# Performance work log

Hardware: AMD Instinct MI355X
Metric: run time of the kernel (lower is better)

The kernel has to match this reference:

```python
import jax, jax.numpy as jnp
import numpy as np

N_NODES = 100000
N_EDGES = 1200000
C = 64            # hidden_channels == in_channels
HEADS = 4
HEAD_D = C // HEADS
EDGE_D = 16
N_LAYERS = 3
NUM_GRAPHS = 128


def setup_inputs() -> dict:
    key = jax.random.key(0)
    ks = jax.random.split(key, 24)
    x = jax.random.normal(ks[0], (N_NODES, C), dtype=jnp.float32)
    edge_index = jax.random.randint(ks[1], (2, N_EDGES), 0, N_NODES, dtype=jnp.int64)
    edge_attr = jax.random.normal(ks[2], (N_EDGES, EDGE_D), dtype=jnp.float32)
    batch = jnp.sort(jax.random.randint(ks[3], (N_NODES,), 0, NUM_GRAPHS, dtype=jnp.int64))
    s = 1.0 / np.sqrt(C)
    se = 1.0 / np.sqrt(EDGE_D)
    inp = {
        "x": x, "edge_index": edge_index, "edge_attr": edge_attr, "batch": batch,
        "Wq": jax.random.normal(ks[4], (N_LAYERS, C, C), jnp.float32) * s,
        "bq": jnp.zeros((N_LAYERS, C), jnp.float32),
        "Wk": jax.random.normal(ks[5], (N_LAYERS, C, C), jnp.float32) * s,
        "bk": jnp.zeros((N_LAYERS, C), jnp.float32),
        "Wv": jax.random.normal(ks[6], (N_LAYERS, C, C), jnp.float32) * s,
        "bv": jnp.zeros((N_LAYERS, C), jnp.float32),
        "We": jax.random.normal(ks[7], (N_LAYERS, EDGE_D, C), jnp.float32) * se,
        "be": jnp.zeros((N_LAYERS, C), jnp.float32),
        "Wskip": jax.random.normal(ks[8], (N_LAYERS, C, C), jnp.float32) * s,
        "bskip": jnp.zeros((N_LAYERS, C), jnp.float32),
        "lin1_w": jax.random.normal(ks[9], (C, C), jnp.float32) * s,
        "lin1_b": jnp.zeros((C,), jnp.float32),
        "lin2_w": jax.random.normal(ks[10], (C, 1), jnp.float32) * s,
        "lin2_b": jnp.zeros((1,), jnp.float32),
    }
    return inp


def _transformer_conv(x, src, dst, edge_attr, Wq, bq, Wk, bk, Wv, bv, We, be, Ws, bs):
    """PyG-style TransformerConv: edge-softmax attention with edge features."""
    n = x.shape[0]
    e = src.shape[0]
    q = (x @ Wq + bq)[dst].reshape(e, HEADS, HEAD_D)          # query at target i
    ea = (edge_attr @ We + be).reshape(e, HEADS, HEAD_D)      # shared edge proj
    k = (x @ Wk + bk)[src].reshape(e, HEADS, HEAD_D) + ea
    v = (x @ Wv + bv)[src].reshape(e, HEADS, HEAD_D) + ea
    logit = jnp.einsum('ehd,ehd->eh', q, k) / jnp.sqrt(jnp.float32(HEAD_D))  # [E,H]
    # numerically-stable softmax over edges sharing the same destination node
    m = jax.ops.segment_max(logit, dst, num_segments=n)       # [N,H]
    ex = jnp.exp(logit - m[dst])
    denom = jax.ops.segment_sum(ex, dst, num_segments=n)      # [N,H]
    alpha = ex / jnp.maximum(denom[dst], 1e-16)
    agg = jax.ops.segment_sum(alpha[:, :, None] * v, dst, num_segments=n)   # [N,H,D]
    return agg.reshape(n, HEADS * HEAD_D) + x @ Ws + bs       # root/skip weight


def reference(x, edge_index, edge_attr, batch, Wq, bq, Wk, bk, Wv, bv, We, be,
              Wskip, bskip, lin1_w, lin1_b, lin2_w, lin2_b):
    src, dst = edge_index[0], edge_index[1]
    h = x
    for l in range(N_LAYERS):
        h = _transformer_conv(h, src, dst, edge_attr,
                              Wq[l], bq[l], Wk[l], bk[l], Wv[l], bv[l],
                              We[l], be[l], Wskip[l], bskip[l])
        if l < N_LAYERS - 1:
            h = jax.nn.relu(h)
    # global mean pool over graphs
    sums = jax.ops.segment_sum(h, batch, num_segments=NUM_GRAPHS)            # [G,C]
    cnt = jax.ops.segment_sum(jnp.ones((h.shape[0], 1), h.dtype), batch,
                              num_segments=NUM_GRAPHS)
    pooled = sums / jnp.maximum(cnt, 1.0)
    out = jax.nn.relu(pooled @ lin1_w + lin1_b)
    return (out @ lin2_w + lin2_b).squeeze(-1)                               # [G]
```

## Files before the change

kernel.cpp:

```cpp
#include <hip/hip_runtime.h>
#include <hip/hip_bf16.h>

#define NODES_C 64
#define HEADS 4
#define HEAD_D 16

__global__ void count_k(const int* __restrict__ dst, int E, int* __restrict__ deg) {
    int e = blockIdx.x * blockDim.x + threadIdx.x;
    if (e < E) atomicAdd(&deg[dst[e]], 1);
}

__global__ __launch_bounds__(1024) void scan_chunk(const int* __restrict__ deg,
                                                   int* __restrict__ excl,
                                                   int* __restrict__ chunkSums, int N) {
    __shared__ int buf[1024];
    int i = blockIdx.x * 1024 + threadIdx.x;
    int v = (i < N) ? deg[i] : 0;
    buf[threadIdx.x] = v;
    __syncthreads();
    for (int off = 1; off < 1024; off <<= 1) {
        int t = (threadIdx.x >= off) ? buf[threadIdx.x - off] : 0;
        __syncthreads();
        buf[threadIdx.x] += t;
        __syncthreads();
    }
    if (i < N) excl[i] = buf[threadIdx.x] - v;
    if (threadIdx.x == 1023) chunkSums[blockIdx.x] = buf[1023];
}

__global__ __launch_bounds__(128) void scan_sums(int* __restrict__ chunkSums, int nChunks) {
    __shared__ int buf[128];
    int v = (threadIdx.x < nChunks) ? chunkSums[threadIdx.x] : 0;
    buf[threadIdx.x] = v;
    __syncthreads();
    for (int off = 1; off < 128; off <<= 1) {
        int t = (threadIdx.x >= off) ? buf[threadIdx.x - off] : 0;
        __syncthreads();
        buf[threadIdx.x] += t;
        __syncthreads();
    }
    if (threadIdx.x < nChunks) chunkSums[threadIdx.x] = buf[threadIdx.x] - v;
}

__global__ void scan_add(int* __restrict__ excl, const int* __restrict__ chunkSums,
                         int N, int E) {
    int i = blockIdx.x * blockDim.x + threadIdx.x;
    if (i < N) excl[i] += chunkSums[i >> 10];
    if (i == 0) excl[N] = E;
}

__global__ void fill_k(const int* __restrict__ dst, int E,
                       const int* __restrict__ row_start, int* __restrict__ cursor,
                       int* __restrict__ csr) {
    int e = blockIdx.x * blockDim.x + threadIdx.x;
    if (e < E) {
        int d = dst[e];
        int pos = atomicAdd(&cursor[d], 1);
        csr[row_start[d] + pos] = e;
    }
}

__global__ void gather_edges(const int* __restrict__ csr, const int* __restrict__ srcA,
                             const float4* __restrict__ ea4,
                             int* __restrict__ csr_src, float4* __restrict__ csr_ea,
                             int E) {
    int t = blockIdx.x * blockDim.x + threadIdx.x;
    int p = t >> 2, q = t & 3;
    if (p < E) {
        int e = csr[p];
        if (q == 0) csr_src[p] = srcA[e];
        csr_ea[(size_t)p * 4 + q] = ea4[(size_t)e * 4 + q];
    }
}

#define GB 16
__global__ __launch_bounds__(256) void gemm_qkvs(
    const float* __restrict__ Hin,
    const float* __restrict__ Wq, const float* __restrict__ bq,
    const float* __restrict__ Wk, const float* __restrict__ bk,
    const float* __restrict__ Wv, const float* __restrict__ bv,
    const float* __restrict__ Ws, const float* __restrict__ bs,
    float* __restrict__ Q, float* __restrict__ KV,
    float* __restrict__ Ssk, int N)
{
    int m = threadIdx.x >> 6;
    int c = threadIdx.x & 63;
    const float* W = (m == 0) ? Wq : (m == 1) ? Wk : (m == 2) ? Wv : Ws;
    const float* b = (m == 0) ? bq : (m == 1) ? bk : (m == 2) ? bv : bs;
    float* Out     = (m == 0) ? Q  : (m == 3) ? Ssk : KV;
    size_t rowStride = (m == 1 || m == 2) ? 128 : 64;
    int cOff = (m == 1) ? 2 * c : (m == 2) ? 2 * c + 1 : c;

    float wcol[64];
#pragma unroll
    for (int t = 0; t < 64; ++t) wcol[t] = W[t * 64 + c];
    float bias = b[c];

    __shared__ __align__(16) float hrow[GB][64];

    for (int base = blockIdx.x * GB; base < N; base += gridDim.x * GB) {
        int nn = min(GB, N - base);
        __syncthreads();
        for (int idx = threadIdx.x; idx < nn * 64; idx += 256)
            hrow[idx >> 6][idx & 63] = Hin[base * 64 + idx];
        __syncthreads();
        for (int r = 0; r < nn; ++r) {
            const float4* h4 = (const float4*)hrow[r];
            float acc = bias;
#pragma unroll
            for (int t4 = 0; t4 < 16; ++t4) {
                float4 hv = h4[t4];
                acc += hv.x * wcol[4 * t4 + 0];
                acc += hv.y * wcol[4 * t4 + 1];
                acc += hv.z * wcol[4 * t4 + 2];
                acc += hv.w * wcol[4 * t4 + 3];
            }
            Out[(size_t)(base + r) * rowStride + cOff] = acc;
        }
    }
}

__global__ __launch_bounds__(256) void attn_pre(
    const float* __restrict__ Q, const float2* __restrict__ KV,
    const float* __restrict__ Ssk,
    const int* __restrict__ row_start, const int* __restrict__ csr_src,
    const float* __restrict__ csr_ea,
    const float* __restrict__ We, const float* __restrict__ be,
    float* __restrict__ Hout, int N, int doRelu)
{
    __shared__ float weS[16 * 68];
    for (int idx = threadIdx.x; idx < 1024; idx += 256)
        weS[(idx >> 6) * 68 + (idx & 63)] = We[idx];
    __syncthreads();

    int lane = threadIdx.x & 63;
    int tl = lane & 15;
    int hb = lane & 48;
    float wcol[16];
#pragma unroll
    for (int t = 0; t < 16; ++t) wcol[t] = weS[t * 68 + lane];
    float beL = be[lane];

    int gwave  = (blockIdx.x * blockDim.x + threadIdx.x) >> 6;
    int nwaves = (gridDim.x * blockDim.x) >> 6;

    for (int i = gwave; i < N; i += nwaves) {
        float q = Q[(size_t)i * 64 + lane];

        const float4* qh4 = (const float4*)(Q + (size_t)i * 64 + hb);
        const float4* wr4 = (const float4*)(weS + tl * 68 + hb);
        float4 qa = qh4[0], qb4 = qh4[1], qc4 = qh4[2], qd = qh4[3];
        float4 wa = wr4[0], wb = wr4[1], wc4 = wr4[2], wd = wr4[3];
        float G = qa.x * wa.x + qa.y * wa.y + qa.z * wa.z + qa.w * wa.w
                + qb4.x * wb.x + qb4.y * wb.y + qb4.z * wb.z + qb4.w * wb.w
                + qc4.x * wc4.x + qc4.y * wc4.y + qc4.z * wc4.z + qc4.w * wc4.w
                + qd.x * wd.x + qd.y * wd.y + qd.z * wd.z + qd.w * wd.w;
        float rb = q * beL;
#pragma unroll
        for (int off = 8; off >= 1; off >>= 1) rb += __shfl_xor(rb, off, 16);
        float qbase = rb * 0.25f;

        int beg = row_start[i], end = row_start[i + 1];
        float m = -INFINITY, s = 0.f, acc = 0.f, z = 0.f;

        int p = beg;
        for (; p + 3 < end; p += 4) {
            int j0 = csr_src[p],     j1 = csr_src[p + 1];
            int j2 = csr_src[p + 2], j3 = csr_src[p + 3];
            float2 kv0 = KV[(size_t)j0 * 64 + lane];
            float2 kv1 = KV[(size_t)j1 * 64 + lane];
            float2 kv2 = KV[(size_t)j2 * 64 + lane];
            float2 kv3 = KV[(size_t)j3 * 64 + lane];
            float a0 = csr_ea[(size_t)p * 16 + tl];
            float a1 = csr_ea[(size_t)p * 16 + 16 + tl];
            float a2 = csr_ea[(size_t)p * 16 + 32 + tl];
            float a3 = csr_ea[(size_t)p * 16 + 48 + tl];

            float l0 = q * kv0.x + a0 * G;
            float l1 = q * kv1.x + a1 * G;
            float l2 = q * kv2.x + a2 * G;
            float l3 = q * kv3.x + a3 * G;
#pragma unroll
            for (int off = 8; off >= 1; off >>= 1) {
                l0 += __shfl_xor(l0, off, 16);
                l1 += __shfl_xor(l1, off, 16);
                l2 += __shfl_xor(l2, off, 16);
                l3 += __shfl_xor(l3, off, 16);
            }
            l0 = l0 * 0.25f + qbase;
            l1 = l1 * 0.25f + qbase;
            l2 = l2 * 0.25f + qbase;
            l3 = l3 * 0.25f + qbase;

            float nm = fmaxf(fmaxf(fmaxf(l0, l1), fmaxf(l2, l3)), m);
            float sc = __expf(m - nm);
            float w0 = __expf(l0 - nm), w1 = __expf(l1 - nm);
            float w2 = __expf(l2 - nm), w3 = __expf(l3 - nm);
            s   = s * sc + w0 + w1 + w2 + w3;
            acc = acc * sc + w0 * kv0.y + w1 * kv1.y + w2 * kv2.y + w3 * kv3.y;
            z   = z * sc + w0 * a0 + w1 * a1 + w2 * a2 + w3 * a3;
            m = nm;
        }
        for (; p < end; ++p) {
            int j = csr_src[p];
            float2 kv = KV[(size_t)j * 64 + lane];
            float a = csr_ea[(size_t)p * 16 + tl];
            float l = q * kv.x + a * G;
#pragma unroll
            for (int off = 8; off >= 1; off >>= 1) l += __shfl_xor(l, off, 16);
            l = l * 0.25f + qbase;
            float nm = fmaxf(m, l);
            float sc = __expf(m - nm);
            float w  = __expf(l - nm);
            s   = s * sc + w;
            acc = acc * sc + w * kv.y;
            z   = z * sc + w * a;
            m = nm;
        }

        float o;
        if (s > 0.f) {
            float t = acc;
#pragma unroll
            for (int u = 0; u < 16; ++u) t += wcol[u] * __shfl(z, u, 16);
            o = t / s + beL + Ssk[(size_t)i * 64 + lane];
        } else {
            o = Ssk[(size_t)i * 64 + lane];
        }
        if (doRelu) o = fmaxf(o, 0.f);
        Hout[(size_t)i * 64 + lane] = o;
    }
}

__global__ __launch_bounds__(256) void attn_k(
    const float* __restrict__ Q, const float2* __restrict__ KV,
    const float* __restrict__ Ssk,
    const int* __restrict__ row_start, const int* __restrict__ csr,
    const int* __restrict__ srcA, const float* __restrict__ edge_attr,
    const float* __restrict__ We, const float* __restrict__ be,
    float* __restrict__ Hout, int N, int doRelu)
{
    int lane = threadIdx.x & 63;
    float wcol[16];
#pragma unroll
    for (int t = 0; t < 16; ++t) wcol[t] = We[t * 64 + lane];
    float beL = be[lane];

    int gwave  = (blockIdx.x * blockDim.x + threadIdx.x) >> 6;
    int nwaves = (gridDim.x * blockDim.x) >> 6;

    for (int i = gwave; i < N; i += nwaves) {
        float q = Q[(size_t)i * 64 + lane];
        int beg = row_start[i], end = row_start[i + 1];
        float m = -INFINITY, s = 0.f, acc = 0.f;
        for (int p = beg; p < end; ++p) {
            int e = csr[p];
            int j = srcA[e];
            const float4* ap = (const float4*)(edge_attr + (size_t)e * 16);
            float4 a0 = ap[0], a1 = ap[1], a2 = ap[2], a3 = ap[3];
            float2 kvp = KV[(size_t)j * 64 + lane];
            float ea = beL;
            ea += a0.x * wcol[0]  + a0.y * wcol[1]  + a0.z * wcol[2]  + a0.w * wcol[3];
            ea += a1.x * wcol[4]  + a1.y * wcol[5]  + a1.z * wcol[6]  + a1.w * wcol[7];
            ea += a2.x * wcol[8]  + a2.y * wcol[9]  + a2.z * wcol[10] + a2.w * wcol[11];
            ea += a3.x * wcol[12] + a3.y * wcol[13] + a3.z * wcol[14] + a3.w * wcol[15];
            float kv = kvp.x + ea, vv = kvp.y + ea;
            float part = q * kv;
#pragma unroll
            for (int off = 8; off >= 1; off >>= 1) part += __shfl_xor(part, off, 16);
            float logit = part * 0.25f;
            float nm = fmaxf(m, logit);
            float sc = __expf(m - nm);
            float w  = __expf(logit - nm);
            s = s * sc + w;  acc = acc * sc + w * vv;  m = nm;
        }
        float agg = (s > 0.f) ? acc / s : 0.f;
        float o = agg + Ssk[(size_t)i * 64 + lane];
        if (doRelu) o = fmaxf(o, 0.f);
        Hout[(size_t)i * 64 + lane] = o;
    }
}

#define POOL_CHUNK 128
__global__ __launch_bounds__(64) void pool_k(
    const float* __restrict__ H, const int* __restrict__ batch,
    float* __restrict__ pooled, float* __restrict__ cnt, int N)
{
    int lane = threadIdx.x;
    int beg = blockIdx.x * POOL_CHUNK;
    if (beg >= N) return;
    int end = min(beg + POOL_CHUNK, N);

    int curg = batch[beg];
    float acc = 0.f, c = 0.f;
    for (int i = beg; i < end; ++i) {
        int g = batch[i];
        if (g != curg) {
            atomicAdd(&pooled[curg * 64 + lane], acc);
            if (lane == 0) atomicAdd(&cnt[curg], c);
            acc = 0.f; c = 0.f; curg = g;
        }
        acc += H[(size_t)i * 64 + lane];
        c += 1.0f;
    }
    atomicAdd(&pooled[curg * 64 + lane], acc);
    if (lane == 0) atomicAdd(&cnt[curg], c);
}

__global__ __launch_bounds__(64) void mlp_k(
    const float* __restrict__ pooled, const float* __restrict__ cnt,
    const float* __restrict__ lin1_w, const float* __restrict__ lin1_b,
    const float* __restrict__ lin2_w, const float* __restrict__ lin2_b,
    float* __restrict__ out)
{
    int g = blockIdx.x;
    int c = threadIdx.x;
    float inv = 1.0f / fmaxf(cnt[g], 1.0f);
    float acc = lin1_b[c];
#pragma unroll
    for (int t = 0; t < 64; ++t) acc += pooled[g * 64 + t] * inv * lin1_w[t * 64 + c];
    float r = fmaxf(acc, 0.f) * lin2_w[c];
#pragma unroll
    for (int off = 32; off >= 1; off >>= 1) r += __shfl_xor(r, off, 64);
    if (c == 0) out[g] = r + lin2_b[0];
}

extern "C" void kernel_launch(void* const* d_in, const int* in_sizes, int n_in,
                              void* d_out, int out_size, void* d_ws, size_t ws_size,
                              hipStream_t stream) {
    const float* x        = (const float*)d_in[0];
    const int*   eidx     = (const int*)  d_in[1];
    const float* eattr    = (const float*)d_in[2];
    const int*   batch    = (const int*)  d_in[3];
    const float* Wq       = (const float*)d_in[4];
    const float* bq       = (const float*)d_in[5];
    const float* Wk       = (const float*)d_in[6];
    const float* bk       = (const float*)d_in[7];
    const float* Wv       = (const float*)d_in[8];
    const float* bv       = (const float*)d_in[9];
    const float* We       = (const float*)d_in[10];
    const float* be       = (const float*)d_in[11];
    const float* Wskip    = (const float*)d_in[12];
    const float* bskip    = (const float*)d_in[13];
    const float* lin1_w   = (const float*)d_in[14];
    const float* lin1_b   = (const float*)d_in[15];
    const float* lin2_w   = (const float*)d_in[16];
    const float* lin2_b   = (const float*)d_in[17];

    int N = in_sizes[0] / 64;
    int E = in_sizes[1] / 2;
    const int* src = eidx;
    const int* dst = eidx + E;

    char* w = (char*)d_ws;
    auto alloc = [&](size_t bytes) {
        char* p = w;
        w += (bytes + 255) & ~(size_t)255;
        return p;
    };
    float* Q   = (float*)alloc((size_t)N * 64 * 4);
    float* KV  = (float*)alloc((size_t)N * 128 * 4);
    float* S   = (float*)alloc((size_t)N * 64 * 4);
    float* H   = (float*)alloc((size_t)N * 64 * 4);
    int* deg       = (int*)alloc((size_t)N * 4);
    int* row_start = (int*)alloc((size_t)(N + 1) * 4);
    int* cursor    = (int*)alloc((size_t)N * 4);
    int* csr       = (int*)alloc((size_t)E * 4);
    int* chunkSums = (int*)alloc(128 * 4);
    float* pooled  = (float*)alloc(128 * 64 * 4);
    float* cnt     = (float*)alloc(128 * 4);
    int*    csr_src = (int*)   alloc((size_t)E * 4);
    float4* csr_ea  = (float4*)alloc((size_t)E * 16 * 4);
    bool pre = ((size_t)(w - (char*)d_ws) <= ws_size);

    hipMemsetAsync(deg, 0, (size_t)N * 4, stream);
    hipMemsetAsync(cursor, 0, (size_t)N * 4, stream);
    hipMemsetAsync(pooled, 0, 128 * 64 * 4, stream);
    hipMemsetAsync(cnt, 0, 128 * 4, stream);

    count_k<<<(E + 255) / 256, 256, 0, stream>>>(dst, E, deg);
    int nChunks = (N + 1023) / 1024;
    scan_chunk<<<nChunks, 1024, 0, stream>>>(deg, row_start, chunkSums, N);
    scan_sums<<<1, 128, 0, stream>>>(chunkSums, nChunks);
    scan_add<<<(N + 255) / 256, 256, 0, stream>>>(row_start, chunkSums, N, E);
    fill_k<<<(E + 255) / 256, 256, 0, stream>>>(dst, E, row_start, cursor, csr);

    if (pre) {
        gather_edges<<<((size_t)E * 4 + 255) / 256, 256, 0, stream>>>(
            csr, src, (const float4*)eattr, csr_src, csr_ea, E);
    }

    const float* Hin = x;
    for (int l = 0; l < 3; ++l) {
        gemm_qkvs<<<1024, 256, 0, stream>>>(Hin,
            Wq + l * 4096, bq + l * 64, Wk + l * 4096, bk + l * 64,
            Wv + l * 4096, bv + l * 64, Wskip + l * 4096, bskip + l * 64,
            Q, KV, S, N);
        if (pre) {
            attn_pre<<<4096, 256, 0, stream>>>(Q, (const float2*)KV, S,
                row_start, csr_src, (const float*)csr_ea,
                We + l * 1024, be + l * 64, H, N, (l < 2) ? 1 : 0);
        } else {
            attn_k<<<4096, 256, 0, stream>>>(Q, (const float2*)KV, S,
                row_start, csr, src, eattr,
                We + l * 1024, be + l * 64, H, N, (l < 2) ? 1 : 0);
        }
        Hin = H;
    }

    int poolBlocks = (N + POOL_CHUNK - 1) / POOL_CHUNK;
    pool_k<<<poolBlocks, 64, 0, stream>>>(Hin, batch, pooled, cnt, N);
    mlp_k<<<128, 64, 0, stream>>>(pooled, cnt, lin1_w, lin1_b, lin2_w, lin2_b,
                                  (float*)d_out);
}
```

Before: 1.064 ms.

## Sort CSR rows and replace atomic pooling with per-graph binary-search mean

Adds a per-row insertion sort of CSR edge ids so each row is in edge-index order, which makes the summation order deterministic and may improve locality in gather_edges. Replaces the chunked atomic pool kernel with one block per graph that binary-searches the sorted batch array, reduces in shared memory and divides by the count directly. This drops two memsets and the atomics. It also hoists the loop-invariant We row loads in attn_pre out of the node loop. The sort adds an extra launch and serial per-thread work on rows of about 12 edges.

```diff
diff --git a/kernel.cpp b/kernel.cpp
--- a/kernel.cpp
+++ b/kernel.cpp
@@ -57,6 +57,19 @@
         int d = dst[e];
         int pos = atomicAdd(&cursor[d], 1);
         csr[row_start[d] + pos] = e;
+    }
+}
+
+__global__ void sort_rows_k(const int* __restrict__ row_start, int* __restrict__ csr,
+                            int N) {
+    int i = blockIdx.x * blockDim.x + threadIdx.x;
+    if (i >= N) return;
+    int beg = row_start[i], end = row_start[i + 1];
+    for (int p = beg + 1; p < end; ++p) {
+        int key = csr[p];
+        int j = p - 1;
+        while (j >= beg && csr[j] > key) { csr[j + 1] = csr[j]; --j; }
+        csr[j + 1] = key;
     }
 }
 
@@ -144,13 +157,14 @@
     int gwave  = (blockIdx.x * blockDim.x + threadIdx.x) >> 6;
     int nwaves = (gridDim.x * blockDim.x) >> 6;
 
+    const float4* wr4 = (const float4*)(weS + tl * 68 + hb);
+    float4 wa = wr4[0], wb = wr4[1], wc4 = wr4[2], wd = wr4[3];
+
     for (int i = gwave; i < N; i += nwaves) {
         float q = Q[(size_t)i * 64 + lane];
 
         const float4* qh4 = (const float4*)(Q + (size_t)i * 64 + hb);
-        const float4* wr4 = (const float4*)(weS + tl * 68 + hb);
         float4 qa = qh4[0], qb4 = qh4[1], qc4 = qh4[2], qd = qh4[3];
-        float4 wa = wr4[0], wb = wr4[1], wc4 = wr4[2], wd = wr4[3];
         float G = qa.x * wa.x + qa.y * wa.y + qa.z * wa.z + qa.w * wa.w
                 + qb4.x * wb.x + qb4.y * wb.y + qb4.z * wb.z + qb4.w * wb.w
                 + qc4.x * wc4.x + qc4.y * wc4.y + qc4.z * wc4.z + qc4.w * wc4.w
@@ -281,44 +295,47 @@
     }
 }
 
-#define POOL_CHUNK 128
-__global__ __launch_bounds__(64) void pool_k(
+__device__ __forceinline__ int lbound(const int* __restrict__ a, int n, int key) {
+    int lo = 0, hi = n;
+    while (lo < hi) { int mid = (lo + hi) >> 1; if (a[mid] < key) lo = mid + 1; else hi = mid; }
+    return lo;
+}
+
+__global__ __launch_bounds__(256) void pool_mean_k(
     const float* __restrict__ H, const int* __restrict__ batch,
-    float* __restrict__ pooled, float* __restrict__ cnt, int N)
+    float* __restrict__ pooled, int N)
 {
-    int lane = threadIdx.x;
-    int beg = blockIdx.x * POOL_CHUNK;
-    if (beg >= N) return;
-    int end = min(beg + POOL_CHUNK, N);
-
-    int curg = batch[beg];
-    float acc = 0.f, c = 0.f;
-    for (int i = beg; i < end; ++i) {
-        int g = batch[i];
-        if (g != curg) {
-            atomicAdd(&pooled[curg * 64 + lane], acc);
-            if (lane == 0) atomicAdd(&cnt[curg], c);
-            acc = 0.f; c = 0.f; curg = g;
-        }
+    int g = blockIdx.x;
+    int lo = lbound(batch, N, g);
+    int hi = lbound(batch, N, g + 1);
+    int lane = threadIdx.x & 63;
+    int w = threadIdx.x >> 6;
+
+    float acc = 0.f;
+    for (int i = lo + w; i < hi; i += 4)
         acc += H[(size_t)i * 64 + lane];
-        c += 1.0f;
-    }
-    atomicAdd(&pooled[curg * 64 + lane], acc);
-    if (lane == 0) atomicAdd(&cnt[curg], c);
+
+    __shared__ float part[4][64];
+    part[w][lane] = acc;
+    __syncthreads();
+    if (w == 0) {
+        float s = ((part[0][lane] + part[1][lane]) + part[2][lane]) + part[3][lane];
+        float cnt = (float)(hi - lo);
+        pooled[g * 64 + lane] = s / fmaxf(cnt, 1.0f);
+    }
 }
 
 __global__ __launch_bounds__(64) void mlp_k(
-    const float* __restrict__ pooled, const float* __restrict__ cnt,
+    const float* __restrict__ pooled,
     const float* __restrict__ lin1_w, const float* __restrict__ lin1_b,
     const float* __restrict__ lin2_w, const float* __restrict__ lin2_b,
     float* __restrict__ out)
 {
     int g = blockIdx.x;
     int c = threadIdx.x;
-    float inv = 1.0f / fmaxf(cnt[g], 1.0f);
     float acc = lin1_b[c];
 #pragma unroll
-    for (int t = 0; t < 64; ++t) acc += pooled[g * 64 + t] * inv * lin1_w[t * 64 + c];
+    for (int t = 0; t < 64; ++t) acc += pooled[g * 64 + t] * lin1_w[t * 64 + c];
     float r = fmaxf(acc, 0.f) * lin2_w[c];
 #pragma unroll
     for (int off = 32; off >= 1; off >>= 1) r += __shfl_xor(r, off, 64);
@@ -368,15 +385,12 @@
     int* csr       = (int*)alloc((size_t)E * 4);
     int* chunkSums = (int*)alloc(128 * 4);
     float* pooled  = (float*)alloc(128 * 64 * 4);
-    float* cnt     = (float*)alloc(128 * 4);
     int*    csr_src = (int*)   alloc((size_t)E * 4);
     float4* csr_ea  = (float4*)alloc((size_t)E * 16 * 4);
     bool pre = ((size_t)(w - (char*)d_ws) <= ws_size);
 
     hipMemsetAsync(deg, 0, (size_t)N * 4, stream);
     hipMemsetAsync(cursor, 0, (size_t)N * 4, stream);
-    hipMemsetAsync(pooled, 0, 128 * 64 * 4, stream);
-    hipMemsetAsync(cnt, 0, 128 * 4, stream);
 
     count_k<<<(E + 255) / 256, 256, 0, stream>>>(dst, E, deg);
     int nChunks = (N + 1023) / 1024;
@@ -384,6 +398,7 @@
     scan_sums<<<1, 128, 0, stream>>>(chunkSums, nChunks);
     scan_add<<<(N + 255) / 256, 256, 0, stream>>>(row_start, chunkSums, N, E);
     fill_k<<<(E + 255) / 256, 256, 0, stream>>>(dst, E, row_start, cursor, csr);
+    sort_rows_k<<<(N + 255) / 256, 256, 0, stream>>>(row_start, csr, N);
 
     if (pre) {
         gather_edges<<<((size_t)E * 4 + 255) / 256, 256, 0, stream>>>(
@@ -408,8 +423,7 @@
         Hin = H;
     }
 
-    int poolBlocks = (N + POOL_CHUNK - 1) / POOL_CHUNK;
-    pool_k<<<poolBlocks, 64, 0, stream>>>(Hin, batch, pooled, cnt, N);
-    mlp_k<<<128, 64, 0, stream>>>(pooled, cnt, lin1_w, lin1_b, lin2_w, lin2_b,
+    pool_mean_k<<<128, 256, 0, stream>>>(Hin, batch, pooled, N);
+    mlp_k<<<128, 64, 0, stream>>>(pooled, lin1_w, lin1_b, lin2_w, lin2_b,
                                   (float*)d_out);
 }
```

Result: slower. 1.087 ms (+2.1%).
